# Optimization experiments

Hardware: AMD Instinct MI355X
Metric: run time of the kernel (lower is better)

Reference implementation:

```python
import jax, jax.numpy as jnp
import numpy as np

N = 50000      # num_nodes
E = 1600000    # num_edges (avg degree 32)
F_IN = 512     # in_features
F_OUT = 64     # out_features
C = 4          # num_cores


def setup_inputs() -> dict:
    key = jax.random.key(0)
    ks = jax.random.split(key, 5)
    x = jax.random.normal(ks[0], (N, F_IN), jnp.float32)
    edge_index = jax.random.randint(ks[1], (2, E), 0, N, dtype=jnp.int32)
    # KokaoCore.signal modeled as tanh(w . v + b) -> scalar, one (w, b) per core
    core_w = jax.random.normal(ks[2], (C, F_IN), jnp.float32) / np.sqrt(F_IN)
    core_b = jnp.zeros((C,), jnp.float32)
    # output_transform: nn.Linear(num_cores, out_features)
    W_out = jax.random.normal(ks[3], (F_OUT, C), jnp.float32) / np.sqrt(C)
    b_out = jnp.zeros((F_OUT,), jnp.float32)
    return {"x": x, "edge_index": edge_index, "core_w": core_w,
            "core_b": core_b, "W_out": W_out, "b_out": b_out}


def reference(x, edge_index, core_w, core_b, W_out, b_out):
    src, tgt = edge_index[0], edge_index[1]
    # per-node, per-core scalar signal (computed once per node, gathered per edge)
    s = jnp.tanh(x @ core_w.T + core_b)                              # (N, C)
    seg_sum = jax.ops.segment_sum(s[src], tgt, num_segments=N)       # (N, C)
    count = jax.ops.segment_sum(jnp.ones((E,), x.dtype), tgt, num_segments=N)  # (N,)
    # mean over neighbors; nodes with no in-edges stay zero (torch.zeros init)
    avg = jnp.where(count[:, None] > 0, seg_sum / jnp.maximum(count, 1.0)[:, None], 0.0)
    # aggregated[i] = avg_signal * x[i][:out_features], stacked over cores on last dim
    messages = avg[:, None, :] * x[:, :F_OUT, None]                  # (N, F_OUT, C)
    out = jnp.einsum('nfc,oc->nfo', messages, W_out) + b_out         # (N, F_OUT, F_OUT)
    return jax.nn.relu(out)
```

## Files before the change

kernel.cpp:

```cpp
#include <hip/hip_runtime.h>

#define F_IN 512
#define F_OUT 64
#define NB_SHIFT 8
#define CAP_B 10240
#define P_CHUNK 4096

typedef float v4f __attribute__((ext_vector_type(4)));
typedef int   v4i __attribute__((ext_vector_type(4)));
typedef unsigned int uint32;


__global__ __launch_bounds__(256) void signal_kernel(
    const float* __restrict__ x, const float* __restrict__ core_w,
    const float* __restrict__ core_b, float* __restrict__ s,
    uint32* __restrict__ gcur, int N, int nb) {
  if (blockIdx.x == 0 && threadIdx.x < (unsigned)nb) gcur[threadIdx.x] = 0;

  int wave = (int)((blockIdx.x * blockDim.x + threadIdx.x) >> 6);
  int lane = threadIdx.x & 63;
  if (wave >= N) return;

  const v4f* xv = (const v4f*)(x + (size_t)wave * F_IN);
  v4f a0 = xv[lane * 2];
  v4f a1 = xv[lane * 2 + 1];

  float p[4];
#pragma unroll
  for (int c = 0; c < 4; ++c) {
    const v4f* wv = (const v4f*)(core_w + c * F_IN);
    v4f w0 = wv[lane * 2];
    v4f w1 = wv[lane * 2 + 1];
    p[c] = a0.x * w0.x + a0.y * w0.y + a0.z * w0.z + a0.w * w0.w +
           a1.x * w1.x + a1.y * w1.y + a1.z * w1.z + a1.w * w1.w;
  }
#pragma unroll
  for (int off = 32; off > 0; off >>= 1) {
#pragma unroll
    for (int c = 0; c < 4; ++c) p[c] += __shfl_down(p[c], off, 64);
  }
  if (lane == 0) {
    v4f r;
    r.x = tanhf(p[0] + core_b[0]);
    r.y = tanhf(p[1] + core_b[1]);
    r.z = tanhf(p[2] + core_b[2]);
    r.w = tanhf(p[3] + core_b[3]);
    ((v4f*)s)[wave] = r;
  }
}

__global__ __launch_bounds__(256) void part_kernel(
    const int* __restrict__ src, const int* __restrict__ tgt,
    uint32* __restrict__ gcur, uint32* __restrict__ grec, int E, int nb) {
  __shared__ uint32 hist[256];
  __shared__ uint32 cur[256];
  int tid = threadIdx.x;
  int start = (int)blockIdx.x * P_CHUNK;

  if (tid < nb) hist[tid] = 0;
  __syncthreads();

  int b[16];
  uint32 rec[16];
#pragma unroll
  for (int j = 0; j < 16; ++j) {
    int i = start + j * 256 + tid;
    b[j] = -1;
    rec[j] = 0;
    if (i < E) {
      int u = src[i];
      int v = tgt[i];
      b[j] = v >> NB_SHIFT;
      rec[j] = (uint32)(v & 255) | ((uint32)u << 8);
      atomicAdd(&hist[b[j]], 1u);
    }
  }
  __syncthreads();
  if (tid < nb) {
    uint32 tot = hist[tid];
    cur[tid] = tot ? atomicAdd(&gcur[tid], tot) : 0u;
  }
  __syncthreads();
#pragma unroll
  for (int j = 0; j < 16; ++j) {
    if (b[j] >= 0) {
      uint32 pos = atomicAdd(&cur[b[j]], 1u);
      if (pos < CAP_B) grec[(size_t)b[j] * CAP_B + pos] = rec[j];
    }
  }
}

__global__ __launch_bounds__(256) void agg_kernel(
    const float* __restrict__ s, const uint32* __restrict__ gcur,
    const uint32* __restrict__ grec, float* __restrict__ avg, int N) {
  int b = blockIdx.x;
  int tid = threadIdx.x;
  __shared__ uint32 acc[256 * 5];

#pragma unroll
  for (int k = 0; k < 5; ++k) acc[tid + k * 256] = 0;
  __syncthreads();

  uint32 cnt = gcur[b];
  if (cnt > CAP_B) cnt = CAP_B;
  const uint32* rp = grec + (size_t)b * CAP_B;
  for (uint32 r = tid; r < cnt; r += 256) {
    uint32 rec = rp[r];
    uint32 node = rec & 255u;
    uint32 u = rec >> 8;
    v4f sv = ((const v4f*)s)[u];
    atomicAdd(&acc[node        ], (uint32)__float2int_rn((sv.x + 1.0f) * 8388608.0f));
    atomicAdd(&acc[node +  256 ], (uint32)__float2int_rn((sv.y + 1.0f) * 8388608.0f));
    atomicAdd(&acc[node +  512 ], (uint32)__float2int_rn((sv.z + 1.0f) * 8388608.0f));
    atomicAdd(&acc[node +  768 ], (uint32)__float2int_rn((sv.w + 1.0f) * 8388608.0f));
    atomicAdd(&acc[node + 1024 ], 1u);
  }
  __syncthreads();

  int n = (b << NB_SHIFT) | tid;
  if (n < N) {
    uint32 deg = acc[tid + 1024];
    float fdeg = (float)deg;
    float inv = deg ? 1.0f / fdeg : 0.0f;
    v4f a;
    a.x = ((float)acc[tid       ] * 0x1p-23f - fdeg) * inv;
    a.y = ((float)acc[tid +  256] * 0x1p-23f - fdeg) * inv;
    a.z = ((float)acc[tid +  512] * 0x1p-23f - fdeg) * inv;
    a.w = ((float)acc[tid +  768] * 0x1p-23f - fdeg) * inv;
    ((v4f*)avg)[n] = a;
  }
}

__global__ __launch_bounds__(256) void out_kernel(
    const float* __restrict__ x, const float* __restrict__ avg,
    const float* __restrict__ W_out, const float* __restrict__ b_out,
    float* __restrict__ out, int N) {
  int lane = threadIdx.x & 63;
  int gwave = (int)((blockIdx.x * blockDim.x + threadIdx.x) >> 6);
  int nwaves = (int)((gridDim.x * blockDim.x) >> 6);
  int col = lane & 15;

  v4f w0 = ((const v4f*)W_out)[col * 4 + 0];
  v4f w1 = ((const v4f*)W_out)[col * 4 + 1];
  v4f w2 = ((const v4f*)W_out)[col * 4 + 2];
  v4f w3 = ((const v4f*)W_out)[col * 4 + 3];
  v4f bq = ((const v4f*)b_out)[col];

  for (int n = gwave; n < N; n += nwaves) {
    v4f a = ((const v4f*)avg)[n];

    float t0 = a.x * w0.x + a.y * w0.y + a.z * w0.z + a.w * w0.w;
    float t1 = a.x * w1.x + a.y * w1.y + a.z * w1.z + a.w * w1.w;
    float t2 = a.x * w2.x + a.y * w2.y + a.z * w2.z + a.w * w2.w;
    float t3 = a.x * w3.x + a.y * w3.y + a.z * w3.z + a.w * w3.w;

    float xval = x[(size_t)n * F_IN + lane];

    v4f* ov = (v4f*)(out + (size_t)n * (F_OUT * F_OUT));
#pragma unroll
    for (int it = 0; it < 16; ++it) {
      float xf = __shfl(xval, (lane >> 4) + it * 4, 64);
      v4f r;
      r.x = fmaxf(xf * t0 + bq.x, 0.0f);
      r.y = fmaxf(xf * t1 + bq.y, 0.0f);
      r.z = fmaxf(xf * t2 + bq.z, 0.0f);
      r.w = fmaxf(xf * t3 + bq.w, 0.0f);
      ov[lane + it * 64] = r;
    }
  }
}

extern "C" void kernel_launch(void* const* d_in, const int* in_sizes, int n_in,
                              void* d_out, int out_size, void* d_ws, size_t ws_size,
                              hipStream_t stream) {
  const float* x      = (const float*)d_in[0];
  const int*   eidx   = (const int*)d_in[1];
  const float* core_w = (const float*)d_in[2];
  const float* core_b = (const float*)d_in[3];
  const float* W_out  = (const float*)d_in[4];
  const float* b_out  = (const float*)d_in[5];
  float* out = (float*)d_out;

  const int N = in_sizes[0] / F_IN;
  const int E = in_sizes[1] / 2;
  const int* src = eidx;
  const int* tgt = eidx + E;
  const int nb = (N + 255) >> NB_SHIFT;

  float*  s    = (float*)d_ws;
  float*  avg  = s + (size_t)N * 4;
  uint32* gcur = (uint32*)(avg + (size_t)N * 4);
  uint32* grec = gcur + 256;

  signal_kernel<<<(N + 3) / 4, 256, 0, stream>>>(x, core_w, core_b, s, gcur, N, nb);
  {
    int blocks = (E + P_CHUNK - 1) / P_CHUNK;
    part_kernel<<<blocks, 256, 0, stream>>>(src, tgt, gcur, grec, E, nb);
  }
  agg_kernel<<<nb, 256, 0, stream>>>(s, gcur, grec, avg, N);
  out_kernel<<<2048, 256, 0, stream>>>(x, avg, W_out, b_out, out, N);
}
```

Before: 927.1 us.

## Halve aggregation bucket size and pack per-node accumulators into 64-bit LDS atomics

Buckets now cover 128 target nodes instead of 256, giving twice as many aggregation blocks and more parallelism in the edge-mean stage. The partition kernel switches from register-held records to two streaming passes over 8192-edge chunks. Aggregation packs four quantized signals plus the in-degree into two 64-bit shared-memory atomics per edge instead of five 32-bit ones. The fourth channel drops to lower fixed-point precision to make room for the count, and bucket capacity is halved, which raises the risk of overflow on skewed degree distributions.

```diff
diff --git a/kernel.cpp b/kernel.cpp
--- a/kernel.cpp
+++ b/kernel.cpp
@@ -2,20 +2,23 @@
 
 #define F_IN 512
 #define F_OUT 64
-#define NB_SHIFT 8
-#define CAP_B 10240
-#define P_CHUNK 4096
+#define NB_SHIFT 7
+#define NB_MAX 512
+#define CAP_B 5120
+#define P_CHUNK 8192
 
 typedef float v4f __attribute__((ext_vector_type(4)));
-typedef int   v4i __attribute__((ext_vector_type(4)));
 typedef unsigned int uint32;
+typedef unsigned long long u64;
 
 
 __global__ __launch_bounds__(256) void signal_kernel(
     const float* __restrict__ x, const float* __restrict__ core_w,
     const float* __restrict__ core_b, float* __restrict__ s,
     uint32* __restrict__ gcur, int N, int nb) {
-  if (blockIdx.x == 0 && threadIdx.x < (unsigned)nb) gcur[threadIdx.x] = 0;
+  if (blockIdx.x == 0) {
+    for (int b = threadIdx.x; b < nb; b += 256) gcur[b] = 0;
+  }
 
   int wave = (int)((blockIdx.x * blockDim.x + threadIdx.x) >> 6);
   int lane = threadIdx.x & 63;
@@ -52,41 +55,32 @@
 __global__ __launch_bounds__(256) void part_kernel(
     const int* __restrict__ src, const int* __restrict__ tgt,
     uint32* __restrict__ gcur, uint32* __restrict__ grec, int E, int nb) {
-  __shared__ uint32 hist[256];
-  __shared__ uint32 cur[256];
+  __shared__ uint32 hist[NB_MAX];
+  __shared__ uint32 cur[NB_MAX];
   int tid = threadIdx.x;
   int start = (int)blockIdx.x * P_CHUNK;
-
-  if (tid < nb) hist[tid] = 0;
-  __syncthreads();
-
-  int b[16];
-  uint32 rec[16];
-#pragma unroll
-  for (int j = 0; j < 16; ++j) {
-    int i = start + j * 256 + tid;
-    b[j] = -1;
-    rec[j] = 0;
-    if (i < E) {
-      int u = src[i];
-      int v = tgt[i];
-      b[j] = v >> NB_SHIFT;
-      rec[j] = (uint32)(v & 255) | ((uint32)u << 8);
-      atomicAdd(&hist[b[j]], 1u);
-    }
-  }
-  __syncthreads();
-  if (tid < nb) {
-    uint32 tot = hist[tid];
-    cur[tid] = tot ? atomicAdd(&gcur[tid], tot) : 0u;
-  }
-  __syncthreads();
-#pragma unroll
-  for (int j = 0; j < 16; ++j) {
-    if (b[j] >= 0) {
-      uint32 pos = atomicAdd(&cur[b[j]], 1u);
-      if (pos < CAP_B) grec[(size_t)b[j] * CAP_B + pos] = rec[j];
-    }
+  int end = start + P_CHUNK;
+  if (end > E) end = E;
+
+  for (int b = tid; b < nb; b += 256) hist[b] = 0;
+  __syncthreads();
+
+  for (int i = start + tid; i < end; i += 256)
+    atomicAdd(&hist[(uint32)tgt[i] >> NB_SHIFT], 1u);
+  __syncthreads();
+
+  for (int b = tid; b < nb; b += 256) {
+    uint32 t = hist[b];
+    cur[b] = t ? atomicAdd(&gcur[b], t) : 0u;
+  }
+  __syncthreads();
+
+  for (int i = start + tid; i < end; i += 256) {
+    uint32 v = (uint32)tgt[i];
+    uint32 u = (uint32)src[i];
+    uint32 b = v >> NB_SHIFT;
+    uint32 pos = atomicAdd(&cur[b], 1u);
+    if (pos < CAP_B) grec[(size_t)b * CAP_B + pos] = (v & 127u) | (u << 7);
   }
 }
 
@@ -95,10 +89,10 @@
     const uint32* __restrict__ grec, float* __restrict__ avg, int N) {
   int b = blockIdx.x;
   int tid = threadIdx.x;
-  __shared__ uint32 acc[256 * 5];
-
-#pragma unroll
-  for (int k = 0; k < 5; ++k) acc[tid + k * 256] = 0;
+  __shared__ u64 accA[128];
+  __shared__ u64 accB[128];
+
+  if (tid < 128) { accA[tid] = 0ull; accB[tid] = 0ull; }
   __syncthreads();
 
   uint32 cnt = gcur[b];
@@ -106,27 +100,31 @@
   const uint32* rp = grec + (size_t)b * CAP_B;
   for (uint32 r = tid; r < cnt; r += 256) {
     uint32 rec = rp[r];
-    uint32 node = rec & 255u;
-    uint32 u = rec >> 8;
+    uint32 node = rec & 127u;
+    uint32 u = rec >> 7;
     v4f sv = ((const v4f*)s)[u];
-    atomicAdd(&acc[node        ], (uint32)__float2int_rn((sv.x + 1.0f) * 8388608.0f));
-    atomicAdd(&acc[node +  256 ], (uint32)__float2int_rn((sv.y + 1.0f) * 8388608.0f));
-    atomicAdd(&acc[node +  512 ], (uint32)__float2int_rn((sv.z + 1.0f) * 8388608.0f));
-    atomicAdd(&acc[node +  768 ], (uint32)__float2int_rn((sv.w + 1.0f) * 8388608.0f));
-    atomicAdd(&acc[node + 1024 ], 1u);
+    uint32 q0 = (uint32)__float2int_rn((sv.x + 1.0f) * 8388608.0f);
+    uint32 q1 = (uint32)__float2int_rn((sv.y + 1.0f) * 8388608.0f);
+    uint32 q2 = (uint32)__float2int_rn((sv.z + 1.0f) * 8388608.0f);
+    uint32 q3 = (uint32)__float2int_rn((sv.w + 1.0f) * 131072.0f);
+    atomicAdd(&accA[node], (u64)q0 | ((u64)q1 << 32));
+    atomicAdd(&accB[node], (u64)q2 | ((u64)(q3 | (1u << 25)) << 32));
   }
   __syncthreads();
 
   int n = (b << NB_SHIFT) | tid;
-  if (n < N) {
-    uint32 deg = acc[tid + 1024];
+  if (tid < 128 && n < N) {
+    u64 wa = accA[tid];
+    u64 wb = accB[tid];
+    uint32 deg = (uint32)(wb >> 57);
+    uint32 f3  = (uint32)(wb >> 32) & 0x1ffffffu;
     float fdeg = (float)deg;
     float inv = deg ? 1.0f / fdeg : 0.0f;
     v4f a;
-    a.x = ((float)acc[tid       ] * 0x1p-23f - fdeg) * inv;
-    a.y = ((float)acc[tid +  256] * 0x1p-23f - fdeg) * inv;
-    a.z = ((float)acc[tid +  512] * 0x1p-23f - fdeg) * inv;
-    a.w = ((float)acc[tid +  768] * 0x1p-23f - fdeg) * inv;
+    a.x = ((float)(uint32)wa         * 0x1p-23f - fdeg) * inv;
+    a.y = ((float)(uint32)(wa >> 32) * 0x1p-23f - fdeg) * inv;
+    a.z = ((float)(uint32)wb         * 0x1p-23f - fdeg) * inv;
+    a.w = ((float)f3                 * 0x1p-17f - fdeg) * inv;
     ((v4f*)avg)[n] = a;
   }
 }
@@ -185,12 +183,12 @@
   const int E = in_sizes[1] / 2;
   const int* src = eidx;
   const int* tgt = eidx + E;
-  const int nb = (N + 255) >> NB_SHIFT;
+  const int nb = (N + 127) >> NB_SHIFT;
 
   float*  s    = (float*)d_ws;
   float*  avg  = s + (size_t)N * 4;
   uint32* gcur = (uint32*)(avg + (size_t)N * 4);
-  uint32* grec = gcur + 256;
+  uint32* grec = gcur + NB_MAX;
 
   signal_kernel<<<(N + 3) / 4, 256, 0, stream>>>(x, core_w, core_b, s, gcur, N, nb);
   {
```

Measured after the change: 940.5 us. Within noise of the previous version (+1.4%).
